# Performance work log

Measured on AMD Instinct MI355X. Metric: run time of the kernel, lower is better.

## Reference

```python
import jax, jax.numpy as jnp
import numpy as np

STRIDE = 2

def setup_inputs() -> dict:
    key = jax.random.key(0)
    k1, k2, k3, k4, k5 = jax.random.split(key, 5)
    B, Cin, H, W = 16, 64, 128, 128
    Cout, kh, kw = 64, 3, 3
    oh = ow = 63  # ceil((H - kh + 1) / STRIDE)
    inp = jax.random.normal(k1, (B, Cin, H, W), dtype=jnp.float32)
    fan_in = Cin * kh * kw
    weight = jax.random.normal(k2, (Cout, Cin, kh, kw), dtype=jnp.float32) / np.sqrt(fan_in)
    bias = jax.random.normal(k3, (Cout,), dtype=jnp.float32) * 0.01
    selh = jax.random.randint(k4, (oh, ow), 0, STRIDE, dtype=jnp.int32)
    selw = jax.random.randint(k5, (oh, ow), 0, STRIDE, dtype=jnp.int32)
    return {"input": inp, "weight": weight, "bias": bias, "selh": selh, "selw": selw}


def reference(input, weight, bias, selh, selw):
    # Stochastic downsampled conv: per output pixel (i,j), pick the patch at
    # row i*stride + selh[i,j], col j*stride + selw[i,j], then apply the conv GEMM.
    Cout, Cin, kh, kw = weight.shape
    oh, ow = selh.shape
    # top-left corner of the selected patch for each output pixel
    rng_h = selh + jnp.arange(0, oh * STRIDE, STRIDE, dtype=jnp.int32)[:, None]   # (oh, ow)
    rng_w = selw + jnp.arange(0, ow * STRIDE, STRIDE, dtype=jnp.int32)[None, :]   # (oh, ow)
    # full patch index grids: (oh, ow, kh, kw)
    ih = rng_h[:, :, None, None] + jnp.arange(kh, dtype=jnp.int32)[None, None, :, None]
    iw = rng_w[:, :, None, None] + jnp.arange(kw, dtype=jnp.int32)[None, None, None, :]
    # gather selected im2col patches only (avoids materializing the full unfold)
    patches = input[:, :, ih, iw]  # (B, Cin, oh, ow, kh, kw)
    out = jnp.einsum('bcyxhw,ochw->boyx', patches, weight) + bias[None, :, None, None]
    return out  # (B, Cout, oh, ow)
```

## Files before the change

### kernel.cpp

```cpp
#include <hip/hip_runtime.h>


#define B_    16
#define CIN   64
#define H_    128
#define W_    128
#define COUT  64
#define OH    63
#define OW    63
#define NPIX  (OH * OW)
#define KTOT  (CIN * 9)

typedef short  short8  __attribute__((ext_vector_type(8)));
typedef float  float4v __attribute__((ext_vector_type(4)));

__device__ inline short f2bf(float f) {
    union { float f; unsigned u; } x; x.f = f;
    unsigned r = x.u + 0x7fffu + ((x.u >> 16) & 1u);
    return (short)(r >> 16);
}

__global__ __launch_bounds__(256)
void transpose_nhwc_bf16(const float* __restrict__ in, short* __restrict__ nhwc) {
    __shared__ float T[64 * 65];
    const int tid = threadIdx.x;
    const int w0  = blockIdx.x * 64;
    const int h   = blockIdx.y;
    const int b   = blockIdx.z;

    {
        const int w4 = tid & 15;
        const int cl = tid >> 4;
#pragma unroll
        for (int i = 0; i < 4; ++i) {
            const int c = cl + 16 * i;
            const float4 v = *(const float4*)&in[((b * CIN + c) * H_ + h) * W_ + w0 + 4 * w4];
            T[c * 65 + 4 * w4 + 0] = v.x;
            T[c * 65 + 4 * w4 + 1] = v.y;
            T[c * 65 + 4 * w4 + 2] = v.z;
            T[c * 65 + 4 * w4 + 3] = v.w;
        }
    }
    __syncthreads();
    {
        const int cg = tid & 7;
        const int wl = tid >> 3;
#pragma unroll
        for (int i = 0; i < 2; ++i) {
            const int w = wl + 32 * i;
            short8 v;
#pragma unroll
            for (int t = 0; t < 8; ++t)
                v[t] = f2bf(T[(8 * cg + t) * 65 + w]);
            *(short8*)&nhwc[((b * H_ + h) * W_ + w0 + w) * CIN + 8 * cg] = v;
        }
    }
}

__global__ __launch_bounds__(576)
void transpose_wgt_bf16(const float* __restrict__ wgt, short* __restrict__ wgt_t) {
    const int o = blockIdx.x;
    const int t = threadIdx.x;
    const int c = t / 9;
    const int tap = t - c * 9;
    wgt_t[o * KTOT + tap * CIN + c] = f2bf(wgt[o * KTOT + c * 9 + tap]);
}

#define PIXT  16
#define BT    4
#define LDO   68

__global__ __launch_bounds__(256, 2)
void sconv2davg_mfma(const short* __restrict__ nhwc,
                     const short* __restrict__ wgt_t,
                     const float* __restrict__ bias,
                     const int* __restrict__ selh,
                     const int* __restrict__ selw,
                     float* __restrict__ out) {
    __shared__ __align__(16) short As[9 * 64 * 32];
    __shared__ __align__(16) short Ws[9 * 64 * 32];
    __shared__ int hb_s[PIXT], wb_s[PIXT];

    const int tid = threadIdx.x;
    const int p0  = blockIdx.x * PIXT;
    const int b0  = blockIdx.y * BT;

    if (tid < PIXT) {
        int p = p0 + tid;
        if (p > NPIX - 1) p = NPIX - 1;
        int y = p / OW;
        int x = p - y * OW;
        hb_s[tid] = 2 * y + selh[p];
        wb_s[tid] = 2 * x + selw[p];
    }
    __syncthreads();

    const int ln = tid & 15;
    const int hl = (tid >> 4) & 3;
    const int wv = tid >> 6;

    const int gm  = tid >> 2;
    const int seg = tid & 3;
    const int pl  = gm >> 2;
    const int bl  = gm & 3;
    const int gb  = b0 + bl;
    const int ih0 = hb_s[pl];
    const int iw0 = wb_s[pl];

    float4v acc[4];
#pragma unroll
    for (int j = 0; j < 4; ++j) acc[j] = (float4v){0.f, 0.f, 0.f, 0.f};

    for (int cc = 0; cc < 2; ++cc) {
        const int c0 = cc * 32;

#pragma unroll
        for (int tap = 0; tap < 9; ++tap) {
            const int kh = tap / 3, kw = tap - 3 * (tap / 3);
            const short8 v = *(const short8*)
                &nhwc[((gb * H_ + ih0 + kh) * W_ + iw0 + kw) * CIN + c0 + seg * 8];
            *(short8*)&As[tap * 2048 + gm * 32 + seg * 8] = v;
        }
#pragma unroll
        for (int tap = 0; tap < 9; ++tap) {
            const short8 v = *(const short8*)
                &wgt_t[gm * KTOT + tap * CIN + c0 + seg * 8];
            *(short8*)&Ws[tap * 2048 + gm * 32 + seg * 8] = v;
        }
        __syncthreads();

#pragma unroll
        for (int tap = 0; tap < 9; ++tap) {
            const short8 a = *(const short8*)
                &As[tap * 2048 + (16 * wv + ln) * 32 + hl * 8];
#pragma unroll
            for (int j = 0; j < 4; ++j) {
                const short8 b = *(const short8*)
                    &Ws[tap * 2048 + (16 * j + ln) * 32 + hl * 8];
                acc[j] = __builtin_amdgcn_mfma_f32_16x16x32_bf16(a, b, acc[j], 0, 0, 0);
            }
        }
        __syncthreads();
    }

    float* Ot = (float*)As;
#pragma unroll
    for (int j = 0; j < 4; ++j) {
        const float bv = bias[16 * j + ln];
#pragma unroll
        for (int r = 0; r < 4; ++r)
            Ot[(16 * wv + 4 * hl + r) * LDO + 16 * j + ln] = acc[j][r] + bv;
    }
    __syncthreads();
    {
        const int o  = tid & 63;
        const int b2 = tid >> 6;
        const int rowbase = ((b0 + b2) * COUT + o) * NPIX;
#pragma unroll
        for (int pp = 0; pp < PIXT; ++pp) {
            const int p = p0 + pp;
            if (p < NPIX)
                out[rowbase + p] = Ot[(pp * 4 + b2) * LDO + o];
        }
    }
}

#define FKC   72
#define FLDA  76
__global__ __launch_bounds__(256, 4)
void sconv2davg_fallback(const float* __restrict__ in,
                         const float* __restrict__ wgt,
                         const float* __restrict__ bias,
                         const int* __restrict__ selh,
                         const int* __restrict__ selw,
                         float* __restrict__ out) {
    __shared__ float As[64 * FLDA];
    __shared__ float Ws[64 * FLDA];
    __shared__ int hb_s[4], wb_s[4];
    const int tid = threadIdx.x;
    const int p0  = blockIdx.x * 4;
    if (tid < 4) {
        int p = p0 + tid;
        if (p > NPIX - 1) p = NPIX - 1;
        int y = p / OW;
        int x = p - y * OW;
        hb_s[tid] = 2 * y + selh[p];
        wb_s[tid] = 2 * x + selw[p];
    }
    __syncthreads();
    const int tn = tid & 15, tm = tid >> 4;
    float acc[4][4];
#pragma unroll
    for (int i = 0; i < 4; ++i)
#pragma unroll
        for (int j = 0; j < 4; ++j) acc[i][j] = 0.0f;
    for (int cc = 0; cc < 8; ++cc) {
        const int c0 = cc * 8;
#pragma unroll
        for (int it = 0; it < 18; ++it) {
            int idx = tid + it * 256;
            int m = idx / FKC, rem = idx - m * FKC;
            int cl = rem / 9, r = rem - cl * 9;
            int kh = r / 3, kw = r - kh * 3;
            As[m * FLDA + rem] =
                in[((((m & 15) * CIN) + (c0 + cl)) * H_ + hb_s[m >> 4] + kh) * W_ + wb_s[m >> 4] + kw];
        }
#pragma unroll
        for (int it = 0; it < 18; ++it) {
            int idx = tid + it * 256;
            int o = idx / FKC, kk = idx - o * FKC;
            Ws[o * FLDA + kk] = wgt[o * KTOT + cc * FKC + kk];
        }
        __syncthreads();
#pragma unroll 2
        for (int k0 = 0; k0 < FKC; k0 += 4) {
            float4 a[4], w[4];
#pragma unroll
            for (int i = 0; i < 4; ++i) a[i] = *(const float4*)&As[(4 * tm + i) * FLDA + k0];
#pragma unroll
            for (int j = 0; j < 4; ++j) w[j] = *(const float4*)&Ws[(tn + 16 * j) * FLDA + k0];
#pragma unroll
            for (int i = 0; i < 4; ++i)
#pragma unroll
                for (int j = 0; j < 4; ++j) {
                    acc[i][j] += a[i].x * w[j].x; acc[i][j] += a[i].y * w[j].y;
                    acc[i][j] += a[i].z * w[j].z; acc[i][j] += a[i].w * w[j].w;
                }
        }
        __syncthreads();
    }
    const int p = p0 + (tm >> 2);
    if (p < NPIX) {
#pragma unroll
        for (int i = 0; i < 4; ++i) {
            int b = (tm & 3) * 4 + i;
#pragma unroll
            for (int j = 0; j < 4; ++j)
                out[((b * COUT) + tn + 16 * j) * NPIX + p] = acc[i][j] + bias[tn + 16 * j];
        }
    }
}

extern "C" void kernel_launch(void* const* d_in, const int* in_sizes, int n_in,
                              void* d_out, int out_size, void* d_ws, size_t ws_size,
                              hipStream_t stream) {
    const float* in   = (const float*)d_in[0];
    const float* wgt  = (const float*)d_in[1];
    const float* bias = (const float*)d_in[2];
    const int*   selh = (const int*)d_in[3];
    const int*   selw = (const int*)d_in[4];
    float* out = (float*)d_out;

    const size_t nhwc_elems = (size_t)B_ * H_ * W_ * CIN;
    const size_t need = (nhwc_elems + (size_t)COUT * KTOT) * 2;

    if (ws_size >= need) {
        short* nhwc  = (short*)d_ws;
        short* wgt_t = nhwc + nhwc_elems;
        transpose_nhwc_bf16<<<dim3(W_ / 64, H_, B_), 256, 0, stream>>>(in, nhwc);
        transpose_wgt_bf16<<<COUT, 576, 0, stream>>>(wgt, wgt_t);
        const int ptiles = (NPIX + PIXT - 1) / PIXT;
        sconv2davg_mfma<<<dim3(ptiles, B_ / BT), 256, 0, stream>>>(
            nhwc, wgt_t, bias, selh, selw, out);
    } else {
        sconv2davg_fallback<<<(NPIX + 3) / 4, 256, 0, stream>>>(
            in, wgt, bias, selh, selw, out);
    }
}
```

Before: 141.7 us.

## Load MFMA operands directly from global memory, dropping LDS staging

The conv kernel no longer stages the im2col patch tile and the weight tile in shared memory. Each lane loads its short8 A and B fragments straight from the NHWC bf16 buffer and the transposed weights, and computes its own patch coordinates from selh/selw. This removes the LDS round trip, the barriers and the large shared footprint, so the launch bound rises to 4 blocks per SM for more occupancy. In exchange, weight fragments are re-read from global/L2 by every wave with no reuse through LDS, and the A loads are less coalesced.

```diff
diff --git a/kernel.cpp b/kernel.cpp
--- a/kernel.cpp
+++ b/kernel.cpp
@@ -70,80 +70,57 @@
 #define BT    4
 #define LDO   68
 
-__global__ __launch_bounds__(256, 2)
+__global__ __launch_bounds__(256, 4)
 void sconv2davg_mfma(const short* __restrict__ nhwc,
                      const short* __restrict__ wgt_t,
                      const float* __restrict__ bias,
                      const int* __restrict__ selh,
                      const int* __restrict__ selw,
                      float* __restrict__ out) {
-    __shared__ __align__(16) short As[9 * 64 * 32];
-    __shared__ __align__(16) short Ws[9 * 64 * 32];
-    __shared__ int hb_s[PIXT], wb_s[PIXT];
+    __shared__ float Ot[64 * LDO];
 
     const int tid = threadIdx.x;
     const int p0  = blockIdx.x * PIXT;
     const int b0  = blockIdx.y * BT;
 
-    if (tid < PIXT) {
-        int p = p0 + tid;
-        if (p > NPIX - 1) p = NPIX - 1;
-        int y = p / OW;
-        int x = p - y * OW;
-        hb_s[tid] = 2 * y + selh[p];
-        wb_s[tid] = 2 * x + selw[p];
-    }
-    __syncthreads();
-
     const int ln = tid & 15;
     const int hl = (tid >> 4) & 3;
     const int wv = tid >> 6;
 
-    const int gm  = tid >> 2;
-    const int seg = tid & 3;
-    const int pl  = gm >> 2;
-    const int bl  = gm & 3;
-    const int gb  = b0 + bl;
-    const int ih0 = hb_s[pl];
-    const int iw0 = wb_s[pl];
+    const int m  = 16 * wv + ln;
+    const int pl = m >> 2;
+    const int bl = m & 3;
+    int p = p0 + pl;
+    if (p > NPIX - 1) p = NPIX - 1;
+    const int y = p / OW;
+    const int x = p - y * OW;
+    const int ih0 = 2 * y + selh[p];
+    const int iw0 = 2 * x + selw[p];
+
+    const short* __restrict__ arow =
+        nhwc + (((size_t)(b0 + bl) * H_ + ih0) * W_ + iw0) * CIN;
+    const short* __restrict__ wrow = wgt_t + (size_t)ln * KTOT;
 
     float4v acc[4];
 #pragma unroll
     for (int j = 0; j < 4; ++j) acc[j] = (float4v){0.f, 0.f, 0.f, 0.f};
 
+#pragma unroll
     for (int cc = 0; cc < 2; ++cc) {
-        const int c0 = cc * 32;
-
+        const int co = cc * 32 + hl * 8;
 #pragma unroll
         for (int tap = 0; tap < 9; ++tap) {
             const int kh = tap / 3, kw = tap - 3 * (tap / 3);
-            const short8 v = *(const short8*)
-                &nhwc[((gb * H_ + ih0 + kh) * W_ + iw0 + kw) * CIN + c0 + seg * 8];
-            *(short8*)&As[tap * 2048 + gm * 32 + seg * 8] = v;
-        }
-#pragma unroll
-        for (int tap = 0; tap < 9; ++tap) {
-            const short8 v = *(const short8*)
-                &wgt_t[gm * KTOT + tap * CIN + c0 + seg * 8];
-            *(short8*)&Ws[tap * 2048 + gm * 32 + seg * 8] = v;
-        }
-        __syncthreads();
-
-#pragma unroll
-        for (int tap = 0; tap < 9; ++tap) {
-            const short8 a = *(const short8*)
-                &As[tap * 2048 + (16 * wv + ln) * 32 + hl * 8];
+            const short8 a = *(const short8*)&arow[(kh * W_ + kw) * CIN + co];
 #pragma unroll
             for (int j = 0; j < 4; ++j) {
                 const short8 b = *(const short8*)
-                    &Ws[tap * 2048 + (16 * j + ln) * 32 + hl * 8];
+                    &wrow[(size_t)(16 * j) * KTOT + tap * CIN + co];
                 acc[j] = __builtin_amdgcn_mfma_f32_16x16x32_bf16(a, b, acc[j], 0, 0, 0);
             }
         }
-        __syncthreads();
-    }
-
-    float* Ot = (float*)As;
+    }
+
 #pragma unroll
     for (int j = 0; j < 4; ++j) {
         const float bv = bias[16 * j + ln];
@@ -158,9 +135,9 @@
         const int rowbase = ((b0 + b2) * COUT + o) * NPIX;
 #pragma unroll
         for (int pp = 0; pp < PIXT; ++pp) {
-            const int p = p0 + pp;
-            if (p < NPIX)
-                out[rowbase + p] = Ot[(pp * 4 + b2) * LDO + o];
+            const int pw = p0 + pp;
+            if (pw < NPIX)
+                out[rowbase + pw] = Ot[(pp * 4 + b2) * LDO + o];
         }
     }
 }
```

New measurement: 164.4 us. 1.16x slower.
